# Kernel tuning notes

Measured on AMD Instinct MI355X. Metric: run time of the kernel, lower is better.

Reference implementation:

```python
import jax, jax.numpy as jnp
import numpy as np

NUM_GRAPHS = 2048  # graph.batch_size
EPS = 1e-6


def setup_inputs() -> dict:
    key = jax.random.key(0)
    k1, k2 = jax.random.split(key)
    N, D = 1000000, 128
    feat = jax.random.normal(k1, (N, D), dtype=jnp.float32)
    segment_ids = jnp.sort(jax.random.randint(k2, (N,), 0, NUM_GRAPHS)).astype(jnp.int64)
    weight = jnp.ones((D,), dtype=jnp.float32)
    bias = jnp.zeros((D,), dtype=jnp.float32)
    mean_scale = jnp.ones((D,), dtype=jnp.float32)
    return {"feat": feat, "segment_ids": segment_ids, "weight": weight,
            "bias": bias, "mean_scale": mean_scale}


def reference(feat, segment_ids, weight, bias, mean_scale):
    # counts per graph ( == graph.batch_num_nodes() ). Clamp to 1 so that
    # empty segments (which never contribute to the output) don't produce NaNs.
    counts = jnp.maximum(
        jax.ops.segment_sum(jnp.ones_like(segment_ids, dtype=feat.dtype),
                            segment_ids, num_segments=NUM_GRAPHS), 1.0)
    inv_counts = (1.0 / counts)[:, None]                      # [B, 1]

    # per-graph mean: scatter_add then divide by segment size
    mean = jax.ops.segment_sum(feat, segment_ids, num_segments=NUM_GRAPHS) * inv_counts  # [B, D]
    sub = feat - mean[segment_ids] * mean_scale               # [N, D]

    # per-graph std of the mean-shifted features
    var = jax.ops.segment_sum(sub * sub, segment_ids, num_segments=NUM_GRAPHS) * inv_counts
    std = jnp.sqrt(var + EPS)                                 # [B, D]

    return weight * sub / std[segment_ids] + bias
```

## Files before the change

kernel.cpp:

```cpp
#include <hip/hip_runtime.h>

#define D 128
#define NSEG 2048
#define EPSV 1e-6f
#define BLOCK 512
#define CPR 32
#define RG (BLOCK/CPR)
#define WAVES (BLOCK/64)

typedef float f32x4 __attribute__((ext_vector_type(4)));

#define ACC(v, sum, sq) { (sum) += (v); (sq) += (v) * (v); }

__global__ __launch_bounds__(BLOCK) void graphnorm_fused(
    const float* __restrict__ feat,
    const int* __restrict__ seg,
    const float* __restrict__ weight,
    const float* __restrict__ bias,
    const float* __restrict__ mean_scale,
    float* __restrict__ out,
    int N)
{
    const int s = blockIdx.x;
    __shared__ int s_range[2];
    __shared__ f32x4 s_sum[WAVES][CPR];
    __shared__ f32x4 s_sq[WAVES][CPR];
    __shared__ f32x4 s_a[CPR];
    __shared__ f32x4 s_b[CPR];

    const int t = threadIdx.x;

    if (t < 2) {
        int target = s + t;
        int lo = 0, hi = N;
        while (lo < hi) {
            int mid = (lo + hi) >> 1;
            if (seg[mid] < target) lo = mid + 1; else hi = mid;
        }
        s_range[t] = lo;
    }
    __syncthreads();
    const int start = s_range[0];
    const int end   = s_range[1];

    const int c = t & (CPR - 1);
    const int g = t >> 5;

    const f32x4* feat4 = reinterpret_cast<const f32x4*>(feat);
    f32x4* out4 = reinterpret_cast<f32x4*>(out);

    f32x4 s0 = 0.f, s1 = 0.f, s2 = 0.f, s3 = 0.f;
    f32x4 q0 = 0.f, q1 = 0.f, q2 = 0.f, q3 = 0.f;

    int r = start + g;
    for (; r + 3 * RG < end; r += 4 * RG) {
        f32x4 v0 = feat4[(r         ) * CPR + c];
        f32x4 v1 = feat4[(r +     RG) * CPR + c];
        f32x4 v2 = feat4[(r + 2 * RG) * CPR + c];
        f32x4 v3 = feat4[(r + 3 * RG) * CPR + c];
        ACC(v0, s0, q0);
        ACC(v1, s1, q1);
        ACC(v2, s2, q2);
        ACC(v3, s3, q3);
    }
    for (; r < end; r += RG) {
        f32x4 v = feat4[r * CPR + c];
        ACC(v, s0, q0);
    }
    s0 += s1; s2 += s3; s0 += s2;
    q0 += q1; q2 += q3; q0 += q2;

    #pragma unroll
    for (int i = 0; i < 4; ++i) {
        s0[i] += __shfl_xor(s0[i], 32);
        q0[i] += __shfl_xor(q0[i], 32);
    }

    const int w    = t >> 6;
    const int lane = t & 63;
    if (lane < 32) {
        s_sum[w][c] = s0;
        s_sq[w][c]  = q0;
    }
    __syncthreads();

    if (t < CPR) {
        f32x4 sm = s_sum[0][t];
        f32x4 sg = s_sq[0][t];
        #pragma unroll
        for (int i = 1; i < WAVES; ++i) {
            sm += s_sum[i][t];
            sg += s_sq[i][t];
        }
        const float cnt = (float)max(end - start, 1);
        const float inv = 1.0f / cnt;
        const f32x4 wv  = reinterpret_cast<const f32x4*>(weight)[t];
        const f32x4 bi  = reinterpret_cast<const f32x4*>(bias)[t];
        const f32x4 msc = reinterpret_cast<const f32x4*>(mean_scale)[t];
        f32x4 A, B;
        #pragma unroll
        for (int i = 0; i < 4; ++i) {
            float mean = sm[i] * inv;
            float ms   = mean * msc[i];
            float var  = fmaxf(sg[i] * inv - 2.f * mean * ms + ms * ms, 0.f);
            float istd = rsqrtf(var + EPSV);
            A[i] = wv[i] * istd;
            B[i] = bi[i] - A[i] * ms;
        }
        s_a[t] = A;
        s_b[t] = B;
    }
    __syncthreads();

    const f32x4 A = s_a[c];
    const f32x4 B = s_b[c];

    r = start + g;
    for (; r + 3 * RG < end; r += 4 * RG) {
        const int i0 = (r         ) * CPR + c;
        const int i1 = (r +     RG) * CPR + c;
        const int i2 = (r + 2 * RG) * CPR + c;
        const int i3 = (r + 3 * RG) * CPR + c;
        f32x4 v0 = feat4[i0];
        f32x4 v1 = feat4[i1];
        f32x4 v2 = feat4[i2];
        f32x4 v3 = feat4[i3];
        __builtin_nontemporal_store(A * v0 + B, &out4[i0]);
        __builtin_nontemporal_store(A * v1 + B, &out4[i1]);
        __builtin_nontemporal_store(A * v2 + B, &out4[i2]);
        __builtin_nontemporal_store(A * v3 + B, &out4[i3]);
    }
    for (; r < end; r += RG) {
        const int idx = r * CPR + c;
        f32x4 v = feat4[idx];
        __builtin_nontemporal_store(A * v + B, &out4[idx]);
    }
}

extern "C" void kernel_launch(void* const* d_in, const int* in_sizes, int n_in,
                              void* d_out, int out_size, void* d_ws, size_t ws_size,
                              hipStream_t stream) {
    const float* feat       = (const float*)d_in[0];
    const int*   seg        = (const int*)d_in[1];
    const float* weight     = (const float*)d_in[2];
    const float* bias       = (const float*)d_in[3];
    const float* mean_scale = (const float*)d_in[4];
    float* out = (float*)d_out;

    const int N = in_sizes[0] / D;

    graphnorm_fused<<<NSEG, BLOCK, 0, stream>>>(
        feat, seg, weight, bias, mean_scale, out, N);
}
```

Before: 238.2 us.

## Cache each segment's rows in registers to avoid re-reading features in normalize pass

Each thread now loads up to 32 row vectors of its segment into a register array and keeps them there. Both the statistics pass and the normalize-and-store pass use those registers, so `feat` is read from global memory only once instead of twice. Rows beyond the 32-row buffer fall back to a tail loop that re-reads from memory. The launch bound now requests two blocks per CU, but the 128-register buffer is tight under that budget and may force spills or cut occupancy.

```diff
diff --git a/kernel.cpp b/kernel.cpp
--- a/kernel.cpp
+++ b/kernel.cpp
@@ -7,12 +7,11 @@
 #define CPR 32
 #define RG (BLOCK/CPR)
 #define WAVES (BLOCK/64)
+#define MAXK 32
 
 typedef float f32x4 __attribute__((ext_vector_type(4)));
 
-#define ACC(v, sum, sq) { (sum) += (v); (sq) += (v) * (v); }
-
-__global__ __launch_bounds__(BLOCK) void graphnorm_fused(
+__global__ __launch_bounds__(BLOCK, 2) void graphnorm_fused(
     const float* __restrict__ feat,
     const int* __restrict__ seg,
     const float* __restrict__ weight,
@@ -49,26 +48,29 @@
     const f32x4* feat4 = reinterpret_cast<const f32x4*>(feat);
     f32x4* out4 = reinterpret_cast<f32x4*>(out);
 
-    f32x4 s0 = 0.f, s1 = 0.f, s2 = 0.f, s3 = 0.f;
-    f32x4 q0 = 0.f, q1 = 0.f, q2 = 0.f, q3 = 0.f;
+    f32x4 buf[MAXK];
+    #pragma unroll
+    for (int k = 0; k < MAXK; ++k) {
+        const int r = start + g + k * RG;
+        if (r < end) buf[k] = feat4[r * CPR + c];
+    }
 
-    int r = start + g;
-    for (; r + 3 * RG < end; r += 4 * RG) {
-        f32x4 v0 = feat4[(r         ) * CPR + c];
-        f32x4 v1 = feat4[(r +     RG) * CPR + c];
-        f32x4 v2 = feat4[(r + 2 * RG) * CPR + c];
-        f32x4 v3 = feat4[(r + 3 * RG) * CPR + c];
-        ACC(v0, s0, q0);
-        ACC(v1, s1, q1);
-        ACC(v2, s2, q2);
-        ACC(v3, s3, q3);
+    f32x4 s0 = 0.f, q0 = 0.f;
+    #pragma unroll
+    for (int k = 0; k < MAXK; ++k) {
+        const int r = start + g + k * RG;
+        if (r < end) {
+            s0 += buf[k];
+            q0 += buf[k] * buf[k];
+        }
     }
-    for (; r < end; r += RG) {
+
+    const int tail_base = start + g + MAXK * RG;
+    for (int r = tail_base; r < end; r += RG) {
         f32x4 v = feat4[r * CPR + c];
-        ACC(v, s0, q0);
+        s0 += v;
+        q0 += v * v;
     }
-    s0 += s1; s2 += s3; s0 += s2;
-    q0 += q1; q2 += q3; q0 += q2;
 
     #pragma unroll
     for (int i = 0; i < 4; ++i) {
@@ -115,25 +117,15 @@
     const f32x4 A = s_a[c];
     const f32x4 B = s_b[c];
 
-    r = start + g;
-    for (; r + 3 * RG < end; r += 4 * RG) {
-        const int i0 = (r         ) * CPR + c;
-        const int i1 = (r +     RG) * CPR + c;
-        const int i2 = (r + 2 * RG) * CPR + c;
-        const int i3 = (r + 3 * RG) * CPR + c;
-        f32x4 v0 = feat4[i0];
-        f32x4 v1 = feat4[i1];
-        f32x4 v2 = feat4[i2];
-        f32x4 v3 = feat4[i3];
-        __builtin_nontemporal_store(A * v0 + B, &out4[i0]);
-        __builtin_nontemporal_store(A * v1 + B, &out4[i1]);
-        __builtin_nontemporal_store(A * v2 + B, &out4[i2]);
-        __builtin_nontemporal_store(A * v3 + B, &out4[i3]);
+    #pragma unroll
+    for (int k = 0; k < MAXK; ++k) {
+        const int r = start + g + k * RG;
+        if (r < end)
+            __builtin_nontemporal_store(A * buf[k] + B, &out4[r * CPR + c]);
     }
-    for (; r < end; r += RG) {
-        const int idx = r * CPR + c;
-        f32x4 v = feat4[idx];
-        __builtin_nontemporal_store(A * v + B, &out4[idx]);
+    for (int r = tail_base; r < end; r += RG) {
+        f32x4 v = feat4[r * CPR + c];
+        __builtin_nontemporal_store(A * v + B, &out4[r * CPR + c]);
     }
 }
 
```

New measurement: 227.5 us. 1.05x faster.
